# Kernel optimization log

Hardware: AMD Instinct MI355X
Metric: run time of the kernel (lower is better)

The kernel has to match this reference:

```python
import jax, jax.numpy as jnp
import numpy as np

B, S, D, H = 2, 2048, 1024, 16
DK = D // H
NEG = -1e9


def setup_inputs() -> dict:
    key = jax.random.key(0)
    ks = jax.random.split(key, 12)
    sc = 1.0 / np.sqrt(D)
    inp = {
        "query": jax.random.normal(ks[0], (B, S, D), jnp.float32),
        "key": jax.random.normal(ks[1], (B, S, D), jnp.float32),
        "value": jax.random.normal(ks[2], (B, S, D), jnp.float32),
        "mask": jnp.ones((B, 1, S), jnp.int32),
        "Wq": jax.random.normal(ks[3], (D, D), jnp.float32) * sc,
        "bq": jnp.zeros((D,), jnp.float32),
        "Wk": jax.random.normal(ks[4], (D, D), jnp.float32) * sc,
        "bk": jnp.zeros((D,), jnp.float32),
        "Wv": jax.random.normal(ks[5], (D, D), jnp.float32) * sc,
        "bv": jnp.zeros((D,), jnp.float32),
        "Wo": jax.random.normal(ks[6], (D, D), jnp.float32) * sc,
        "bo": jnp.zeros((D,), jnp.float32),
    }
    return inp


def reference(query, key, value, mask, Wq, bq, Wk, bk, Wv, bv, Wo, bo):
    # projections + split heads: [B,S,D] -> [B,H,S,DK]
    def proj(x, W, b):
        return (x @ W + b).reshape(B, S, H, DK).transpose(0, 2, 1, 3)

    q = proj(query, Wq, bq)
    k = proj(key, Wk, bk)
    v = proj(value, Wv, bv)

    scores = jnp.einsum("bhqd,bhkd->bhqk", q, k) / jnp.sqrt(jnp.float32(DK))
    # mask: [B,1,S] -> unsqueeze head dim -> [B,1,1,S], broadcast over heads & queries
    m = mask[:, None, :, :]  # [B,1,1,S]
    scores = jnp.where(m == 0, NEG, scores)
    p_attn = jax.nn.softmax(scores, axis=-1)  # dropout p=0 (eval)
    x = jnp.einsum("bhqk,bhkd->bhqd", p_attn, v)
    x = x.transpose(0, 2, 1, 3).reshape(B, S, D)
    return x @ Wo + bo
```

## Files before the change

### kernel.cpp

```cpp
#include <hip/hip_runtime.h>
#include <stdint.h>

typedef unsigned short u16;
typedef __bf16 bf16x8 __attribute__((ext_vector_type(8), may_alias));
typedef unsigned short u16x8 __attribute__((ext_vector_type(8), may_alias));
typedef unsigned short u16x4 __attribute__((ext_vector_type(4), may_alias));
typedef float f32x4 __attribute__((ext_vector_type(4)));
typedef float f32x16 __attribute__((ext_vector_type(16)));
typedef int i32x2 __attribute__((ext_vector_type(2)));

__device__ __forceinline__ u16 f2bf(float f) {
    union { float f; uint32_t i; } v; v.f = f;
    return (u16)((v.i + 0x7FFFu + ((v.i >> 16) & 1u)) >> 16);
}

__device__ __forceinline__ float exp2_hw(float x) {
#if __has_builtin(__builtin_amdgcn_exp2f)
    return __builtin_amdgcn_exp2f(x);
#else
    float r; asm("v_exp_f32 %0, %1" : "=v"(r) : "v"(x)); return r;
#endif
}

__device__ __forceinline__ uint32_t cvt_pk_bf16(float a, float b) {
    uint32_t r;
    asm("v_cvt_pk_bf16_f32 %0, %1, %2" : "=v"(r) : "v"(a), "v"(b));
    return r;
}

__device__ __forceinline__ void pl32swap(uint32_t& a, uint32_t& b) {
#if __has_builtin(__builtin_amdgcn_permlane32_swap)
    i32x2 r = __builtin_amdgcn_permlane32_swap((int)a, (int)b, false, false);
    a = (uint32_t)r[0]; b = (uint32_t)r[1];
#else
    asm("v_permlane32_swap_b32 %0, %1" : "+v"(a), "+v"(b));
#endif
}

__device__ __forceinline__ void gld_lds16(const u16* g, u16* l) {
    __builtin_amdgcn_global_load_lds(
        (const __attribute__((address_space(1))) unsigned int*)g,
        (__attribute__((address_space(3))) unsigned int*)l, 16, 0, 0);
}

__global__ __launch_bounds__(256) void cvt_all(
    const float* __restrict__ s0, const float* __restrict__ s1, const float* __restrict__ s2,
    const float* __restrict__ w0, const float* __restrict__ w1,
    const float* __restrict__ w2, const float* __restrict__ w3,
    u16* __restrict__ d0, u16* __restrict__ d1, u16* __restrict__ d2,
    u16* __restrict__ t0, u16* __restrict__ t1,
    u16* __restrict__ t2, u16* __restrict__ t3)
{
    __shared__ float L[64][65];
    const int z = blockIdx.z;
    const int tid = threadIdx.x;
    if (z < 3) {
        const float* s = (z == 0) ? s0 : (z == 1) ? s1 : s2;
        u16*         d = (z == 0) ? d0 : (z == 1) ? d1 : d2;
        const size_t base = ((size_t)blockIdx.x * 256 + tid) * 16;
        #pragma unroll
        for (int p = 0; p < 2; ++p) {
            float4 a = *reinterpret_cast<const float4*>(s + base + p * 8);
            float4 b = *reinterpret_cast<const float4*>(s + base + p * 8 + 4);
            u16x8 o;
            o[0] = f2bf(a.x); o[1] = f2bf(a.y); o[2] = f2bf(a.z); o[3] = f2bf(a.w);
            o[4] = f2bf(b.x); o[5] = f2bf(b.y); o[6] = f2bf(b.z); o[7] = f2bf(b.w);
            *reinterpret_cast<u16x8*>(d + base + p * 8) = o;
        }
    } else {
        if (blockIdx.x >= 256) return;
        const int zi = z - 3;
        const float* w = (zi == 0) ? w0 : (zi == 1) ? w1 : (zi == 2) ? w2 : w3;
        u16*         t = (zi == 0) ? t0 : (zi == 1) ? t1 : (zi == 2) ? t2 : t3;
        const int k0 = (blockIdx.x & 15) * 64, n0 = (blockIdx.x >> 4) * 64;
        const int rr = tid >> 6, cc = tid & 63;
        #pragma unroll
        for (int p = 0; p < 16; ++p)
            L[p * 4 + rr][cc] = w[(size_t)(k0 + p * 4 + rr) * 1024 + n0 + cc];
        __syncthreads();
        #pragma unroll
        for (int p = 0; p < 16; ++p)
            t[(size_t)(n0 + p * 4 + rr) * 1024 + k0 + cc] = f2bf(L[cc][p * 4 + rr]);
    }
}

__global__ __launch_bounds__(256) void gemm_bt(
    const u16* __restrict__ A0, const u16* __restrict__ A1, const u16* __restrict__ A2,
    const u16* __restrict__ B0, const u16* __restrict__ B1, const u16* __restrict__ B2,
    const float* __restrict__ c0, const float* __restrict__ c1, const float* __restrict__ c2,
    void* __restrict__ d0, void* __restrict__ d1, void* __restrict__ d2,
    int mode_override)
{
    __shared__ u16 As[2 * 4096];
    __shared__ u16 Bs[2 * 4096];

    const int z = blockIdx.z;
    const u16* A = (z == 0) ? A0 : (z == 1) ? A1 : A2;
    const u16* BT = (z == 0) ? B0 : (z == 1) ? B1 : B2;
    const float* bias = (z == 0) ? c0 : (z == 1) ? c1 : c2;
    void* dst = (z == 0) ? d0 : (z == 1) ? d1 : d2;
    const int mode = (mode_override >= 0) ? mode_override : ((z == 2) ? 2 : 0);

    const int tid  = threadIdx.x;
    const int wave = tid >> 6, lane = tid & 63;
    const int quad = lane >> 4, l15 = lane & 15;
    const int row0 = blockIdx.x * 128, col0 = blockIdx.y * 128;
    const int wrow = (wave >> 1) * 64, wcol = (wave & 1) * 64;

    const int sidx0 = tid, sidx1 = 256 + tid;
    const int sr0 = sidx0 >> 2, sc0 = ((sidx0 & 3) ^ ((sr0 >> 1) & 3)) * 8;
    const int sr1 = sidx1 >> 2, sc1 = ((sidx1 & 3) ^ ((sr1 >> 1) & 3)) * 8;
    const size_t aoff0 = (size_t)(row0 + sr0) * 1024 + sc0;
    const size_t aoff1 = (size_t)(row0 + sr1) * 1024 + sc1;
    const size_t boff0 = (size_t)(col0 + sr0) * 1024 + sc0;
    const size_t boff1 = (size_t)(col0 + sr1) * 1024 + sc1;
    u16* const asl0 = &As[(size_t)(wave * 64) * 8];
    u16* const asl1 = &As[(size_t)(256 + wave * 64) * 8];
    u16* const bsl0 = &Bs[(size_t)(wave * 64) * 8];
    u16* const bsl1 = &Bs[(size_t)(256 + wave * 64) * 8];

    f32x4 acc[4][4] = {};

    gld_lds16(A + aoff0, asl0);
    gld_lds16(BT + boff0, bsl0);
    gld_lds16(A + aoff1, asl1);
    gld_lds16(BT + boff1, bsl1);
    __syncthreads();

    int cur = 0;
    for (int k0 = 0; k0 < 1024; k0 += 32) {
        if (k0 < 992) {
            const int nb = (cur ^ 1) * 4096;
            gld_lds16(A + aoff0 + (k0 + 32), asl0 + nb);
            gld_lds16(BT + boff0 + (k0 + 32), bsl0 + nb);
            gld_lds16(A + aoff1 + (k0 + 32), asl1 + nb);
            gld_lds16(BT + boff1 + (k0 + 32), bsl1 + nb);
        }

        const u16* Ab = &As[cur * 4096];
        const u16* Bb = &Bs[cur * 4096];
        bf16x8 a[4], b[4];
        #pragma unroll
        for (int i = 0; i < 4; ++i) {
            const int ar = wrow + i * 16 + l15;
            a[i] = *reinterpret_cast<const bf16x8*>(&Ab[ar * 32 + (quad ^ ((ar >> 1) & 3)) * 8]);
        }
        #pragma unroll
        for (int j = 0; j < 4; ++j) {
            const int br = wcol + j * 16 + l15;
            b[j] = *reinterpret_cast<const bf16x8*>(&Bb[br * 32 + (quad ^ ((br >> 1) & 3)) * 8]);
        }
        #pragma unroll
        for (int i = 0; i < 4; ++i)
            #pragma unroll
            for (int j = 0; j < 4; ++j)
                acc[i][j] = __builtin_amdgcn_mfma_f32_16x16x32_bf16(a[i], b[j], acc[i][j], 0, 0, 0);

        __syncthreads();
        cur ^= 1;
    }

    const float emul = (mode == 0 && z == 0 && mode_override < 0) ? 0.18033688011112042f : 1.0f;

    #pragma unroll
    for (int i = 0; i < 4; ++i) {
        #pragma unroll
        for (int j = 0; j < 4; ++j) {
            const int gc  = col0 + wcol + j * 16 + l15;
            const float bv = bias[gc];
            const int gr0 = row0 + wrow + i * 16 + quad * 4;
            if (mode == 3) {
                float* df = (float*)dst;
                #pragma unroll
                for (int r = 0; r < 4; ++r)
                    df[(size_t)(gr0 + r) * 1024 + gc] = acc[i][j][r] + bv;
            } else if (mode == 2) {
                u16* dp = (u16*)dst;
                const int b = gr0 >> 11, s = gr0 & 2047;
                const int h = gc >> 6,  dk = gc & 63;
                u16x4 pk;
                pk[0] = f2bf(acc[i][j][0] + bv);
                pk[1] = f2bf(acc[i][j][1] + bv);
                pk[2] = f2bf(acc[i][j][2] + bv);
                pk[3] = f2bf(acc[i][j][3] + bv);
                *reinterpret_cast<u16x4*>(dp + ((size_t)((b * 16 + h) * 64 + dk)) * 2048 + s) = pk;
            } else {
                u16* dp = (u16*)dst;
                #pragma unroll
                for (int r = 0; r < 4; ++r) {
                    const int gr = gr0 + r;
                    const int b = gr >> 11, s = gr & 2047;
                    const int h = gc >> 6, dk = gc & 63;
                    dp[((size_t)((b * 16 + h) * 2048 + s)) * 64 + dk] = f2bf((acc[i][j][r] + bv) * emul);
                }
            }
        }
    }
}

__global__ __launch_bounds__(512, 4) void attn_fused(
    const u16* __restrict__ Qb, const u16* __restrict__ Kb,
    const u16* __restrict__ Vt, const int* __restrict__ mask,
    u16* __restrict__ ctx)
{
    __shared__ __align__(16) u16 SMEM[16896];

    const int tid  = threadIdx.x;
    const int w    = tid >> 6;
    const int lane = tid & 63;
    const int l31  = lane & 31;
    const int hi   = lane >> 5;
    const int qw   = w & 3;
    const int kh   = w >> 2;

    const int id = blockIdx.x;
    const int sw = (id & 7) * 64 + (id >> 3);
    const int bh = sw >> 4;
    const int q0 = (sw & 15) * 128;
    const int b  = bh >> 4, h = bh & 15;

    const u16* Qp = Qb + (size_t)bh * 2048 * 64;
    const u16* Kp = Kb + (size_t)bh * 2048 * 64;
    const u16* Vp = Vt + (size_t)bh * 64 * 2048;
    const int* mp = mask + b * 2048;

    bf16x8 qf[4];
    {
        const u16* qrow = Qp + (size_t)(q0 + qw * 32 + l31) * 64 + hi * 8;
        #pragma unroll
        for (int s = 0; s < 4; ++s)
            qf[s] = *reinterpret_cast<const bf16x8*>(qrow + s * 16);
    }

    const u16* kgs = Kp + (size_t)(lane ^ w) * 64 + w * 8;
    const u16* vgs = Vp + (size_t)(lane ^ w) * 2048 + w * 8;

    gld_lds16(kgs, &SMEM[w * 512]);
    gld_lds16(vgs, &SMEM[4096 + w * 512]);
    int mreg = mp[lane];
    __syncthreads();

    f32x16 accO0 = {}, accO1 = {};
    float la0 = 0.f, la1 = 0.f, la2 = 0.f, la3 = 0.f;

    int cur = 0;
    for (int t = 0; t < 32; ++t) {
        const int kk = t * 64;
        int mnext = 1;
        if (t < 31) {
            const int nb = (cur ^ 1) * 8192;
            gld_lds16(kgs + (size_t)(kk + 64) * 64, &SMEM[nb + w * 512]);
            gld_lds16(vgs + (kk + 64), &SMEM[nb + 4096 + w * 512]);
            mnext = mp[kk + 64 + lane];
        }
        const u16* Kb_ = &SMEM[cur * 8192];
        const u16* Vb_ = &SMEM[cur * 8192 + 4096];

        const bool fullmask = (__ballot(mreg != 0) == ~0ull);

        f32x16 z = {};
        __builtin_amdgcn_s_setprio(1);
        #pragma unroll
        for (int s = 0; s < 4; ++s) {
            const int cb = s * 2 + hi;
            const bf16x8 ak = *reinterpret_cast<const bf16x8*>(
                &Kb_[cb * 512 + (((kh * 32 + l31)) ^ cb) * 8]);
            z = __builtin_amdgcn_mfma_f32_32x32x16_bf16(ak, qf[s], z, 0, 0, 0);
        }
        __builtin_amdgcn_s_setprio(0);
        float p[16];
        #pragma unroll
        for (int r = 0; r < 16; ++r) p[r] = exp2_hw(z[r]);
        if (!fullmask) {
            #pragma unroll
            for (int r = 0; r < 16; ++r) {
                const int kv = kk + kh * 32 + (r & 3) + 8 * (r >> 2) + 4 * hi;
                if (mp[kv] == 0) p[r] = 0.f;
            }
        }
        la0 += p[0] + p[4] + p[8]  + p[12];
        la1 += p[1] + p[5] + p[9]  + p[13];
        la2 += p[2] + p[6] + p[10] + p[14];
        la3 += p[3] + p[7] + p[11] + p[15];

        uint32_t wd0 = cvt_pk_bf16(p[0],  p[1]);
        uint32_t wd1 = cvt_pk_bf16(p[2],  p[3]);
        uint32_t wd2 = cvt_pk_bf16(p[4],  p[5]);
        uint32_t wd3 = cvt_pk_bf16(p[6],  p[7]);
        uint32_t wd4 = cvt_pk_bf16(p[8],  p[9]);
        uint32_t wd5 = cvt_pk_bf16(p[10], p[11]);
        uint32_t wd6 = cvt_pk_bf16(p[12], p[13]);
        uint32_t wd7 = cvt_pk_bf16(p[14], p[15]);
        pl32swap(wd0, wd2);
        pl32swap(wd1, wd3);
        pl32swap(wd4, wd6);
        pl32swap(wd5, wd7);
        union { uint32_t u[4]; bf16x8 v; } A0, A1;
        A0.u[0] = wd0; A0.u[1] = wd1; A0.u[2] = wd2; A0.u[3] = wd3;
        A1.u[0] = wd4; A1.u[1] = wd5; A1.u[2] = wd6; A1.u[3] = wd7;

        const int ck0 = kh * 4 + hi;
        const int ck1 = kh * 4 + 2 + hi;
        const bf16x8 bv00 = *reinterpret_cast<const bf16x8*>(&Vb_[ck0 * 512 + ((     l31) ^ ck0) * 8]);
        const bf16x8 bv01 = *reinterpret_cast<const bf16x8*>(&Vb_[ck1 * 512 + ((     l31) ^ ck1) * 8]);
        const bf16x8 bv10 = *reinterpret_cast<const bf16x8*>(&Vb_[ck0 * 512 + ((32 + l31) ^ ck0) * 8]);
        const bf16x8 bv11 = *reinterpret_cast<const bf16x8*>(&Vb_[ck1 * 512 + ((32 + l31) ^ ck1) * 8]);
        __builtin_amdgcn_s_setprio(1);
        accO0 = __builtin_amdgcn_mfma_f32_32x32x16_bf16(A0.v, bv00, accO0, 0, 0, 0);
        accO0 = __builtin_amdgcn_mfma_f32_32x32x16_bf16(A1.v, bv01, accO0, 0, 0, 0);
        accO1 = __builtin_amdgcn_mfma_f32_32x32x16_bf16(A0.v, bv10, accO1, 0, 0, 0);
        accO1 = __builtin_amdgcn_mfma_f32_32x32x16_bf16(A1.v, bv11, accO1, 0, 0, 0);
        __builtin_amdgcn_s_setprio(0);

        __syncthreads();
        cur ^= 1;
        mreg = mnext;
    }

    float l_part = (la0 + la1) + (la2 + la3);
    l_part += __shfl_xor(l_part, 32);
    float* F = (float*)SMEM;
    if (kh) {
        #pragma unroll
        for (int r = 0; r < 16; ++r) F[qw * 1024 + r * 64 + lane] = accO0[r];
        #pragma unroll
        for (int r = 0; r < 16; ++r) F[4096 + qw * 1024 + r * 64 + lane] = accO1[r];
        if (lane < 32) F[8192 + qw * 32 + l31] = l_part;
    }
    __syncthreads();
    if (!kh && lane < 32)
        F[8320 + qw * 32 + l31] = 1.0f / (l_part + F[8192 + qw * 32 + l31]);
    __syncthreads();
    if (!kh) {
        #pragma unroll
        for (int r = 0; r < 16; ++r) {
            const int qr = (r & 3) + 8 * (r >> 2) + 4 * hi;
            const float iv = F[8320 + qw * 32 + qr];
            const float o0 = accO0[r] + F[qw * 1024 + r * 64 + lane];
            const float o1 = accO1[r] + F[4096 + qw * 1024 + r * 64 + lane];
            u16* row = ctx + (size_t)(b * 2048 + q0 + qw * 32 + qr) * 1024 + h * 64;
            row[l31]      = f2bf(o0 * iv);
            row[32 + l31] = f2bf(o1 * iv);
        }
    }
}

extern "C" void kernel_launch(void* const* d_in, const int* in_sizes, int n_in,
                              void* d_out, int out_size, void* d_ws, size_t ws_size,
                              hipStream_t stream) {
    const float* query = (const float*)d_in[0];
    const float* key   = (const float*)d_in[1];
    const float* value = (const float*)d_in[2];
    const int*   mask  = (const int*)d_in[3];
    const float* Wq = (const float*)d_in[4];
    const float* bq = (const float*)d_in[5];
    const float* Wk = (const float*)d_in[6];
    const float* bk = (const float*)d_in[7];
    const float* Wv = (const float*)d_in[8];
    const float* bv = (const float*)d_in[9];
    const float* Wo = (const float*)d_in[10];
    const float* bo = (const float*)d_in[11];
    float* out = (float*)d_out;

    u16* ws   = (u16*)d_ws;
    u16* Xq   = ws;
    u16* Xk   = ws + 4194304;
    u16* Xv   = ws + 8388608;
    u16* WqT  = ws + 12582912;
    u16* WkT  = ws + 13631488;
    u16* WvT  = ws + 14680064;
    u16* WoT  = ws + 15728640;
    u16* Qb   = ws + 16777216;
    u16* Kb   = ws + 20971520;
    u16* Vt   = ws + 25165824;
    u16* ctx  = Xq;

    dim3 blk(256);
    cvt_all<<<dim3(1024, 1, 7), blk, 0, stream>>>(query, key, value, Wq, Wk, Wv, Wo,
                                                  Xq, Xk, Xv, WqT, WkT, WvT, WoT);
    gemm_bt<<<dim3(32, 8, 3),  blk, 0, stream>>>(Xq, Xk, Xv, WqT, WkT, WvT,
                                                 bq, bk, bv, Qb, Kb, Vt, -1);
    attn_fused<<<dim3(512), dim3(512), 0, stream>>>(Qb, Kb, Vt, mask, ctx);
    gemm_bt<<<dim3(32, 8, 1),  blk, 0, stream>>>(ctx, ctx, ctx, WoT, WoT, WoT,
                                                 bo, bo, bo, out, out, out, 3);
}
```

Baseline: 226.0 us.

## Process two 64-key tiles per iteration to halve barrier count in attention loop

The attention main loop now stages 128 keys per iteration, two 64-key K/V sub-tiles per buffer, instead of 64. This halves the number of __syncthreads barriers and loop iterations and gives the scheduler two independent QK^T MFMA chains to interleave with the exp work. In exchange, shared memory per block roughly doubles (64 KB vs about 33 KB), which may cut the number of resident blocks per CU, and register pressure rises.

```diff
diff --git a/kernel.cpp b/kernel.cpp
--- a/kernel.cpp
+++ b/kernel.cpp
@@ -203,7 +203,7 @@
     const u16* __restrict__ Vt, const int* __restrict__ mask,
     u16* __restrict__ ctx)
 {
-    __shared__ __align__(16) u16 SMEM[16896];
+    __shared__ __align__(16) u16 SMEM[32768];
 
     const int tid  = threadIdx.x;
     const int w    = tid >> 6;
@@ -235,86 +235,147 @@
     const u16* kgs = Kp + (size_t)(lane ^ w) * 64 + w * 8;
     const u16* vgs = Vp + (size_t)(lane ^ w) * 2048 + w * 8;
 
-    gld_lds16(kgs, &SMEM[w * 512]);
-    gld_lds16(vgs, &SMEM[4096 + w * 512]);
-    int mreg = mp[lane];
+    gld_lds16(kgs,                 &SMEM[w * 512]);
+    gld_lds16(kgs + (size_t)64*64, &SMEM[4096 + w * 512]);
+    gld_lds16(vgs,                 &SMEM[8192 + w * 512]);
+    gld_lds16(vgs + 64,            &SMEM[12288 + w * 512]);
+    int mregA = mp[lane], mregB = mp[64 + lane];
     __syncthreads();
 
     f32x16 accO0 = {}, accO1 = {};
     float la0 = 0.f, la1 = 0.f, la2 = 0.f, la3 = 0.f;
+    const int krd = (kh * 32 + l31);
 
     int cur = 0;
-    for (int t = 0; t < 32; ++t) {
-        const int kk = t * 64;
-        int mnext = 1;
-        if (t < 31) {
-            const int nb = (cur ^ 1) * 8192;
-            gld_lds16(kgs + (size_t)(kk + 64) * 64, &SMEM[nb + w * 512]);
-            gld_lds16(vgs + (kk + 64), &SMEM[nb + 4096 + w * 512]);
-            mnext = mp[kk + 64 + lane];
-        }
-        const u16* Kb_ = &SMEM[cur * 8192];
-        const u16* Vb_ = &SMEM[cur * 8192 + 4096];
-
-        const bool fullmask = (__ballot(mreg != 0) == ~0ull);
-
-        f32x16 z = {};
+    for (int t = 0; t < 16; ++t) {
+        const int kk = t * 128;
+        int mnA = 1, mnB = 1;
+        if (t < 15) {
+            const int nb = (cur ^ 1) * 16384;
+            const int kkn = kk + 128;
+            gld_lds16(kgs + (size_t)kkn * 64,        &SMEM[nb + w * 512]);
+            gld_lds16(kgs + (size_t)(kkn + 64) * 64, &SMEM[nb + 4096 + w * 512]);
+            gld_lds16(vgs + kkn,                     &SMEM[nb + 8192 + w * 512]);
+            gld_lds16(vgs + kkn + 64,                &SMEM[nb + 12288 + w * 512]);
+            mnA = mp[kkn + lane];
+            mnB = mp[kkn + 64 + lane];
+        }
+        const u16* Kb_ = &SMEM[cur * 16384];
+        const u16* Vb_ = &SMEM[cur * 16384 + 8192];
+
+        const bool fullA = (__ballot(mregA != 0) == ~0ull);
+        const bool fullB = (__ballot(mregB != 0) == ~0ull);
+
+        f32x16 zA = {}, zB = {};
         __builtin_amdgcn_s_setprio(1);
         #pragma unroll
         for (int s = 0; s < 4; ++s) {
             const int cb = s * 2 + hi;
             const bf16x8 ak = *reinterpret_cast<const bf16x8*>(
-                &Kb_[cb * 512 + (((kh * 32 + l31)) ^ cb) * 8]);
-            z = __builtin_amdgcn_mfma_f32_32x32x16_bf16(ak, qf[s], z, 0, 0, 0);
+                &Kb_[cb * 512 + (krd ^ cb) * 8]);
+            zA = __builtin_amdgcn_mfma_f32_32x32x16_bf16(ak, qf[s], zA, 0, 0, 0);
+        }
+        #pragma unroll
+        for (int s = 0; s < 4; ++s) {
+            const int cb = s * 2 + hi;
+            const bf16x8 ak = *reinterpret_cast<const bf16x8*>(
+                &Kb_[4096 + cb * 512 + (krd ^ cb) * 8]);
+            zB = __builtin_amdgcn_mfma_f32_32x32x16_bf16(ak, qf[s], zB, 0, 0, 0);
         }
         __builtin_amdgcn_s_setprio(0);
-        float p[16];
-        #pragma unroll
-        for (int r = 0; r < 16; ++r) p[r] = exp2_hw(z[r]);
-        if (!fullmask) {
+
+        {
+            float p[16];
             #pragma unroll
-            for (int r = 0; r < 16; ++r) {
-                const int kv = kk + kh * 32 + (r & 3) + 8 * (r >> 2) + 4 * hi;
-                if (mp[kv] == 0) p[r] = 0.f;
+            for (int r = 0; r < 16; ++r) p[r] = exp2_hw(zA[r]);
+            if (!fullA) {
+                #pragma unroll
+                for (int r = 0; r < 16; ++r) {
+                    const int kv = kk + kh * 32 + (r & 3) + 8 * (r >> 2) + 4 * hi;
+                    if (mp[kv] == 0) p[r] = 0.f;
+                }
             }
-        }
-        la0 += p[0] + p[4] + p[8]  + p[12];
-        la1 += p[1] + p[5] + p[9]  + p[13];
-        la2 += p[2] + p[6] + p[10] + p[14];
-        la3 += p[3] + p[7] + p[11] + p[15];
-
-        uint32_t wd0 = cvt_pk_bf16(p[0],  p[1]);
-        uint32_t wd1 = cvt_pk_bf16(p[2],  p[3]);
-        uint32_t wd2 = cvt_pk_bf16(p[4],  p[5]);
-        uint32_t wd3 = cvt_pk_bf16(p[6],  p[7]);
-        uint32_t wd4 = cvt_pk_bf16(p[8],  p[9]);
-        uint32_t wd5 = cvt_pk_bf16(p[10], p[11]);
-        uint32_t wd6 = cvt_pk_bf16(p[12], p[13]);
-        uint32_t wd7 = cvt_pk_bf16(p[14], p[15]);
-        pl32swap(wd0, wd2);
-        pl32swap(wd1, wd3);
-        pl32swap(wd4, wd6);
-        pl32swap(wd5, wd7);
-        union { uint32_t u[4]; bf16x8 v; } A0, A1;
-        A0.u[0] = wd0; A0.u[1] = wd1; A0.u[2] = wd2; A0.u[3] = wd3;
-        A1.u[0] = wd4; A1.u[1] = wd5; A1.u[2] = wd6; A1.u[3] = wd7;
-
-        const int ck0 = kh * 4 + hi;
-        const int ck1 = kh * 4 + 2 + hi;
-        const bf16x8 bv00 = *reinterpret_cast<const bf16x8*>(&Vb_[ck0 * 512 + ((     l31) ^ ck0) * 8]);
-        const bf16x8 bv01 = *reinterpret_cast<const bf16x8*>(&Vb_[ck1 * 512 + ((     l31) ^ ck1) * 8]);
-        const bf16x8 bv10 = *reinterpret_cast<const bf16x8*>(&Vb_[ck0 * 512 + ((32 + l31) ^ ck0) * 8]);
-        const bf16x8 bv11 = *reinterpret_cast<const bf16x8*>(&Vb_[ck1 * 512 + ((32 + l31) ^ ck1) * 8]);
-        __builtin_amdgcn_s_setprio(1);
-        accO0 = __builtin_amdgcn_mfma_f32_32x32x16_bf16(A0.v, bv00, accO0, 0, 0, 0);
-        accO0 = __builtin_amdgcn_mfma_f32_32x32x16_bf16(A1.v, bv01, accO0, 0, 0, 0);
-        accO1 = __builtin_amdgcn_mfma_f32_32x32x16_bf16(A0.v, bv10, accO1, 0, 0, 0);
-        accO1 = __builtin_amdgcn_mfma_f32_32x32x16_bf16(A1.v, bv11, accO1, 0, 0, 0);
-        __builtin_amdgcn_s_setprio(0);
+            la0 += p[0] + p[4] + p[8]  + p[12];
+            la1 += p[1] + p[5] + p[9]  + p[13];
+            la2 += p[2] + p[6] + p[10] + p[14];
+            la3 += p[3] + p[7] + p[11] + p[15];
+            uint32_t wd0 = cvt_pk_bf16(p[0],  p[1]);
+            uint32_t wd1 = cvt_pk_bf16(p[2],  p[3]);
+            uint32_t wd2 = cvt_pk_bf16(p[4],  p[5]);
+            uint32_t wd3 = cvt_pk_bf16(p[6],  p[7]);
+            uint32_t wd4 = cvt_pk_bf16(p[8],  p[9]);
+            uint32_t wd5 = cvt_pk_bf16(p[10], p[11]);
+            uint32_t wd6 = cvt_pk_bf16(p[12], p[13]);
+            uint32_t wd7 = cvt_pk_bf16(p[14], p[15]);
+            pl32swap(wd0, wd2);
+            pl32swap(wd1, wd3);
+            pl32swap(wd4, wd6);
+            pl32swap(wd5, wd7);
+            union { uint32_t u[4]; bf16x8 v; } A0, A1;
+            A0.u[0] = wd0; A0.u[1] = wd1; A0.u[2] = wd2; A0.u[3] = wd3;
+            A1.u[0] = wd4; A1.u[1] = wd5; A1.u[2] = wd6; A1.u[3] = wd7;
+            const int ck0 = kh * 4 + hi;
+            const int ck1 = kh * 4 + 2 + hi;
+            const bf16x8 bv00 = *reinterpret_cast<const bf16x8*>(&Vb_[ck0 * 512 + ((     l31) ^ ck0) * 8]);
+            const bf16x8 bv01 = *reinterpret_cast<const bf16x8*>(&Vb_[ck1 * 512 + ((     l31) ^ ck1) * 8]);
+            const bf16x8 bv10 = *reinterpret_cast<const bf16x8*>(&Vb_[ck0 * 512 + ((32 + l31) ^ ck0) * 8]);
+            const bf16x8 bv11 = *reinterpret_cast<const bf16x8*>(&Vb_[ck1 * 512 + ((32 + l31) ^ ck1) * 8]);
+            __builtin_amdgcn_s_setprio(1);
+            accO0 = __builtin_amdgcn_mfma_f32_32x32x16_bf16(A0.v, bv00, accO0, 0, 0, 0);
+            accO0 = __builtin_amdgcn_mfma_f32_32x32x16_bf16(A1.v, bv01, accO0, 0, 0, 0);
+            accO1 = __builtin_amdgcn_mfma_f32_32x32x16_bf16(A0.v, bv10, accO1, 0, 0, 0);
+            accO1 = __builtin_amdgcn_mfma_f32_32x32x16_bf16(A1.v, bv11, accO1, 0, 0, 0);
+            __builtin_amdgcn_s_setprio(0);
+        }
+
+        {
+            float p[16];
+            #pragma unroll
+            for (int r = 0; r < 16; ++r) p[r] = exp2_hw(zB[r]);
+            if (!fullB) {
+                #pragma unroll
+                for (int r = 0; r < 16; ++r) {
+                    const int kv = kk + 64 + kh * 32 + (r & 3) + 8 * (r >> 2) + 4 * hi;
+                    if (mp[kv] == 0) p[r] = 0.f;
+                }
+            }
+            la0 += p[0] + p[4] + p[8]  + p[12];
+            la1 += p[1] + p[5] + p[9]  + p[13];
+            la2 += p[2] + p[6] + p[10] + p[14];
+            la3 += p[3] + p[7] + p[11] + p[15];
+            uint32_t wd0 = cvt_pk_bf16(p[0],  p[1]);
+            uint32_t wd1 = cvt_pk_bf16(p[2],  p[3]);
+            uint32_t wd2 = cvt_pk_bf16(p[4],  p[5]);
+            uint32_t wd3 = cvt_pk_bf16(p[6],  p[7]);
+            uint32_t wd4 = cvt_pk_bf16(p[8],  p[9]);
+            uint32_t wd5 = cvt_pk_bf16(p[10], p[11]);
+            uint32_t wd6 = cvt_pk_bf16(p[12], p[13]);
+            uint32_t wd7 = cvt_pk_bf16(p[14], p[15]);
+            pl32swap(wd0, wd2);
+            pl32swap(wd1, wd3);
+            pl32swap(wd4, wd6);
+            pl32swap(wd5, wd7);
+            union { uint32_t u[4]; bf16x8 v; } A0, A1;
+            A0.u[0] = wd0; A0.u[1] = wd1; A0.u[2] = wd2; A0.u[3] = wd3;
+            A1.u[0] = wd4; A1.u[1] = wd5; A1.u[2] = wd6; A1.u[3] = wd7;
+            const int ck0 = kh * 4 + hi;
+            const int ck1 = kh * 4 + 2 + hi;
+            const bf16x8 bv00 = *reinterpret_cast<const bf16x8*>(&Vb_[4096 + ck0 * 512 + ((     l31) ^ ck0) * 8]);
+            const bf16x8 bv01 = *reinterpret_cast<const bf16x8*>(&Vb_[4096 + ck1 * 512 + ((     l31) ^ ck1) * 8]);
+            const bf16x8 bv10 = *reinterpret_cast<const bf16x8*>(&Vb_[4096 + ck0 * 512 + ((32 + l31) ^ ck0) * 8]);
+            const bf16x8 bv11 = *reinterpret_cast<const bf16x8*>(&Vb_[4096 + ck1 * 512 + ((32 + l31) ^ ck1) * 8]);
+            __builtin_amdgcn_s_setprio(1);
+            accO0 = __builtin_amdgcn_mfma_f32_32x32x16_bf16(A0.v, bv00, accO0, 0, 0, 0);
+            accO0 = __builtin_amdgcn_mfma_f32_32x32x16_bf16(A1.v, bv01, accO0, 0, 0, 0);
+            accO1 = __builtin_amdgcn_mfma_f32_32x32x16_bf16(A0.v, bv10, accO1, 0, 0, 0);
+            accO1 = __builtin_amdgcn_mfma_f32_32x32x16_bf16(A1.v, bv11, accO1, 0, 0, 0);
+            __builtin_amdgcn_s_setprio(0);
+        }
 
         __syncthreads();
         cur ^= 1;
-        mreg = mnext;
+        mregA = mnA;
+        mregB = mnB;
     }
 
     float l_part = (la0 + la1) + (la2 + la3);
```

New measurement: 265.9 us. 17.6% more time.
